# Kernel optimization log

Hardware: AMD Instinct MI355X
Metric: run time of the kernel (lower is better)

The kernel has to match this reference:

```python
import jax, jax.numpy as jnp
import numpy as np

B, N, E, T, HID = 8, 2048, 8192, 4096, 128
ALPHA_MAX = 0.05


def setup_inputs() -> dict:
    key = jax.random.key(0)
    k1, k2, k3, k4 = jax.random.split(key, 4)
    H = jax.random.normal(k1, (B, N, HID), dtype=jnp.float32)
    # Incidence-like matrices (dense in the original module)
    B1 = jax.random.normal(k2, (N, E), dtype=jnp.float32) * 0.05
    B2 = jax.random.normal(k3, (E, T), dtype=jnp.float32) * 0.05
    W = jax.random.normal(k4, (HID, HID), dtype=jnp.float32) * (1.0 / np.sqrt(HID))
    alpha_raw = jnp.asarray(-2.5, dtype=jnp.float32)
    return {"H": H, "B1": B1, "B2": B2, "W": W, "alpha_raw": alpha_raw}


def reference(H, B1, B2, W, alpha_raw):
    # diag(L1) = diag(B1^T B1) + diag(B2 B2^T) without forming [E,E]
    L1_diag = jnp.sum(B1 * B1, axis=0) + jnp.sum(B2 * B2, axis=1)  # [E]
    # nodes -> edges (B1_T @ H)
    E_feat = jnp.einsum('ne,bnh->beh', B1, H)          # [B,E,h]
    E_topo = E_feat * L1_diag[None, :, None]            # Laplacian-diag scale
    # edges -> nodes
    dH = jnp.einsum('ne,beh->bnh', B1, E_topo)          # [B,N,h]
    dH = jax.nn.relu(jnp.einsum('bnh,oh->bno', dH, W))  # Linear(no bias) + ReLU
    alpha = ALPHA_MAX * jax.nn.sigmoid(alpha_raw)
    return H + alpha * dH
```

## Files before the change

### kernel.cpp

```cpp
#include <hip/hip_runtime.h>
#include <hip/hip_bf16.h>

typedef unsigned short tcr_u16;
typedef unsigned int   tcr_u32;

enum TcrDims { kB = 8, kN = 2048, kE = 8192, kT = 4096, kHID = 128, kNC = 1024 };

union TcrFU { float f; tcr_u32 u; };

__device__ __forceinline__ float tcr_blo(tcr_u32 w) { TcrFU v; v.u = w << 16;          return v.f; }
__device__ __forceinline__ float tcr_bhi(tcr_u32 w) { TcrFU v; v.u = w & 0xFFFF0000u;  return v.f; }
__device__ __forceinline__ tcr_u16 tcr_f2b(float f) {
    TcrFU v; v.f = f; tcr_u32 x = v.u;
    return (tcr_u16)((x + 0x7FFFu + ((x >> 16) & 1u)) >> 16);
}
__device__ __forceinline__ tcr_u32 tcr_pk2(float lo, float hi) {
    __hip_bfloat16 a = __float2bfloat16(lo);
    __hip_bfloat16 b = __float2bfloat16(hi);
    tcr_u16 ua = *(const tcr_u16*)&a;
    tcr_u16 ub = *(const tcr_u16*)&b;
    return (tcr_u32)ua | ((tcr_u32)ub << 16);
}

struct alignas(8)  TcrU2 { tcr_u32 x, y; };
struct alignas(16) TcrU4 { tcr_u32 x, y, z, w; };
struct alignas(16) TcrF4 { float x, y, z, w; };

typedef __attribute__((ext_vector_type(8))) short bf16x8;
typedef __attribute__((ext_vector_type(4))) float f32x4;

template<int DT>
__device__ __forceinline__ void tcr_load4(const void* p, size_t idx, float* o) {
    if (DT == 0) {
        TcrU2 q = *(const TcrU2*)((const tcr_u16*)p + idx);
        o[0] = tcr_blo(q.x); o[1] = tcr_bhi(q.x);
        o[2] = tcr_blo(q.y); o[3] = tcr_bhi(q.y);
    } else {
        TcrF4 q = *(const TcrF4*)((const float*)p + idx);
        o[0] = q.x; o[1] = q.y; o[2] = q.z; o[3] = q.w;
    }
}

__global__ void TopoCycleResidualNodeAlpha_49641232007243_kernel() {}

__global__ void tcr_probe(const void* Hp, const void* Ap, int* flags) {
    if (blockIdx.x == 0 && threadIdx.x == 0) {
        const tcr_u32* w = (const tcr_u32*)Hp;
        int plausible = 0;
        for (int i = 0; i < 64; ++i) {
            float v = tcr_blo(w[i] & 0xFFFFu);
            float a = fabsf(v);
            if (a >= 0.015625f && a <= 8.0f) plausible++;
        }
        flags[0] = (plausible >= 32) ? 0 : 1;
        tcr_u32 aw = *(const tcr_u32*)Ap;
        flags[1] = (aw == 0xC0200000u) ? 1 : 0;
    }
}

template<int DT>
__global__ void tcr_l1_rowsum(const void* B2, float* L1, const int* flags) {
    if (flags[0] != DT) return;
    int e = blockIdx.x;
    size_t base = (size_t)e * kT;
    int t0 = threadIdx.x * 4;
    float s = 0.f;
    for (int it = 0; it < kT; it += 1024) {
        float v[4];
        tcr_load4<DT>(B2, base + it + t0, v);
        s += v[0] * v[0] + v[1] * v[1] + v[2] * v[2] + v[3] * v[3];
    }
    __shared__ float red[256];
    red[threadIdx.x] = s;
    __syncthreads();
    for (int off = 128; off > 0; off >>= 1) {
        if ((int)threadIdx.x < off) red[threadIdx.x] += red[threadIdx.x + off];
        __syncthreads();
    }
    if (threadIdx.x == 0) L1[e] = red[0];
}

template<int DT>
__global__ void tcr_l1_colsum(const void* B1, float* L1, const int* flags) {
    if (flags[0] != DT) return;
    int e0 = blockIdx.x * 1024 + threadIdx.x * 4;
    int n0 = blockIdx.y * 64;
    float s0 = 0, s1 = 0, s2 = 0, s3 = 0;
    for (int n = n0; n < n0 + 64; ++n) {
        float v[4];
        tcr_load4<DT>(B1, (size_t)n * kE + e0, v);
        s0 += v[0] * v[0]; s1 += v[1] * v[1]; s2 += v[2] * v[2]; s3 += v[3] * v[3];
    }
    atomicAdd(&L1[e0 + 0], s0);
    atomicAdd(&L1[e0 + 1], s1);
    atomicAdd(&L1[e0 + 2], s2);
    atomicAdd(&L1[e0 + 3], s3);
}

struct Reg8 { float f[8]; TcrU2 u0, u1; };

template<int DT>
__device__ __forceinline__ void load_T(const void* src, size_t base, int ld,
                                       Reg8* r, int t) {
    const int k  = (t & 15) * 2;
    const int c0 = (t >> 4) * 8;
    tcr_load4<DT>(src, base + (size_t)k * ld + c0,         r[0].f);
    tcr_load4<DT>(src, base + (size_t)k * ld + c0 + 4,     r[0].f + 4);
    tcr_load4<DT>(src, base + (size_t)(k + 1) * ld + c0,     r[1].f);
    tcr_load4<DT>(src, base + (size_t)(k + 1) * ld + c0 + 4, r[1].f + 4);
}

__device__ __forceinline__ void write_T(tcr_u16 (*dst)[40], const Reg8* r, int t) {
    const int k  = (t & 15) * 2;
    const int c0 = (t >> 4) * 8;
#pragma unroll
    for (int j = 0; j < 8; ++j)
        *(tcr_u32*)&dst[c0 + j][k] = tcr_pk2(r[0].f[j], r[1].f[j]);
}

template<int DT, int ROWS>
__device__ __forceinline__ void load_D(const void* src, size_t base, int ld,
                                       Reg8* r, int t) {
    const int k0 = (t & 3) * 8;
#pragma unroll
    for (int p = 0; p < ROWS / 64; ++p) {
        int m = (t >> 2) + p * 64;
        size_t off = base + (size_t)m * ld + k0;
        if (DT == 0) {
            r[p].u0 = *(const TcrU2*)((const tcr_u16*)src + off);
            r[p].u1 = *(const TcrU2*)((const tcr_u16*)src + off + 4);
        } else {
            tcr_load4<1>(src, off,     r[p].f);
            tcr_load4<1>(src, off + 4, r[p].f + 4);
        }
    }
}

template<int DT, int ROWS>
__device__ __forceinline__ void write_D(tcr_u16 (*dst)[40], const Reg8* r, int t) {
    const int k0 = (t & 3) * 8;
#pragma unroll
    for (int p = 0; p < ROWS / 64; ++p) {
        int m = (t >> 2) + p * 64;
        if (DT == 0) {
            *(TcrU2*)&dst[m][k0]     = r[p].u0;
            *(TcrU2*)&dst[m][k0 + 4] = r[p].u1;
        } else {
            TcrU2 o0, o1;
            o0.x = tcr_pk2(r[p].f[0], r[p].f[1]); o0.y = tcr_pk2(r[p].f[2], r[p].f[3]);
            o1.x = tcr_pk2(r[p].f[4], r[p].f[5]); o1.y = tcr_pk2(r[p].f[6], r[p].f[7]);
            *(TcrU2*)&dst[m][k0]     = o0;
            *(TcrU2*)&dst[m][k0 + 4] = o1;
        }
    }
}

template<int DT>
__global__ __launch_bounds__(256)
void tcr_mm1(const void* B1, const void* H, const float* L1,
             tcr_u16* C1T, const int* flags) {
    if (flags[0] != DT) return;
    __shared__ tcr_u16 As[128][40];
    __shared__ tcr_u16 Bs[128][40];
    const int t  = threadIdx.x;
    const int et = blockIdx.x * 128;
    const int ct = blockIdx.y * 128;
    const int b0 = ct >> 7;
    const int lane = t & 63, w = t >> 6;
    const int mf = lane & 15, q = lane >> 4;
    const int wr = w >> 1, wc = w & 1;

    const f32x4 zero4 = {0.f, 0.f, 0.f, 0.f};
    f32x4 acc[4][4];
#pragma unroll
    for (int i = 0; i < 4; ++i)
#pragma unroll
        for (int j = 0; j < 4; ++j) acc[i][j] = zero4;

    const size_t hbase = (size_t)b0 * ((size_t)kN * kHID);

    Reg8 ra[2], rb[2];
    load_T<DT>(B1, (size_t)0 * kE + et, kE, ra, t);
    load_T<DT>(H,  hbase,               kHID, rb, t);

    for (int kt = 0; kt < kN; kt += 32) {
        write_T(As, ra, t);
        write_T(Bs, rb, t);
        __syncthreads();
        if (kt + 32 < kN) {
            load_T<DT>(B1, (size_t)(kt + 32) * kE + et,        kE,   ra, t);
            load_T<DT>(H,  hbase + (size_t)(kt + 32) * kHID,   kHID, rb, t);
        }
        bf16x8 af[4], bf[4];
#pragma unroll
        for (int i = 0; i < 4; ++i)
            af[i] = *(const bf16x8*)&As[wr * 64 + i * 16 + mf][q * 8];
#pragma unroll
        for (int j = 0; j < 4; ++j)
            bf[j] = *(const bf16x8*)&Bs[wc * 64 + j * 16 + mf][q * 8];
#pragma unroll
        for (int i = 0; i < 4; ++i)
#pragma unroll
            for (int j = 0; j < 4; ++j)
                acc[i][j] = __builtin_amdgcn_mfma_f32_16x16x32_bf16(
                    af[i], bf[j], acc[i][j], 0, 0, 0);
        __syncthreads();
    }

#pragma unroll
    for (int i = 0; i < 4; ++i) {
        const int e0 = et + wr * 64 + i * 16 + q * 4;
        const TcrF4 s = *(const TcrF4*)&L1[e0];
#pragma unroll
        for (int j = 0; j < 4; ++j) {
            const int c = ct + wc * 64 + j * 16 + mf;
            f32x4 a = acc[i][j];
            TcrU2 o;
            o.x = tcr_pk2(a[0] * s.x, a[1] * s.y);
            o.y = tcr_pk2(a[2] * s.z, a[3] * s.w);
            *(TcrU2*)(C1T + (size_t)c * kE + e0) = o;
        }
    }
}

template<int DT>
__global__ __launch_bounds__(256)
void tcr_mm2(const void* B1, const tcr_u16* C1T, tcr_u16* dHp, int kper,
             const int* flags) {
    if (flags[0] != DT) return;
    __shared__ tcr_u16 As[64][40];
    __shared__ tcr_u16 Bs[128][40];
    const int t  = threadIdx.x;
    const int nt = blockIdx.x * 64;
    const int ct = blockIdx.y * 128;
    const int kbase = blockIdx.z * kper;
    const int lane = t & 63, w = t >> 6;
    const int mf = lane & 15, q = lane >> 4;
    const int wr = w >> 1, wc = w & 1;

    const f32x4 zero4 = {0.f, 0.f, 0.f, 0.f};
    f32x4 acc[2][4];
#pragma unroll
    for (int i = 0; i < 2; ++i)
#pragma unroll
        for (int j = 0; j < 4; ++j) acc[i][j] = zero4;

    Reg8 ra[1], rb[2];
    load_D<DT, 64>(B1,  (size_t)nt * kE + kbase, kE, ra, t);
    load_D<0, 128>(C1T, (size_t)ct * kE + kbase, kE, rb, t);

    for (int kt = 0; kt < kper; kt += 32) {
        write_D<DT, 64>(As, ra, t);
        write_D<0, 128>(Bs, rb, t);
        __syncthreads();
        if (kt + 32 < kper) {
            load_D<DT, 64>(B1,  (size_t)nt * kE + kbase + kt + 32, kE, ra, t);
            load_D<0, 128>(C1T, (size_t)ct * kE + kbase + kt + 32, kE, rb, t);
        }
        bf16x8 af[2], bf[4];
#pragma unroll
        for (int i = 0; i < 2; ++i)
            af[i] = *(const bf16x8*)&As[wr * 32 + i * 16 + mf][q * 8];
#pragma unroll
        for (int j = 0; j < 4; ++j)
            bf[j] = *(const bf16x8*)&Bs[wc * 64 + j * 16 + mf][q * 8];
#pragma unroll
        for (int i = 0; i < 2; ++i)
#pragma unroll
            for (int j = 0; j < 4; ++j)
                acc[i][j] = __builtin_amdgcn_mfma_f32_16x16x32_bf16(
                    af[i], bf[j], acc[i][j], 0, 0, 0);
        __syncthreads();
    }

    const int b0 = ct >> 7;
    tcr_u16* op = dHp + (size_t)blockIdx.z * ((size_t)kB * kN * kHID)
                + (size_t)b0 * kN * kHID;
#pragma unroll
    for (int i = 0; i < 2; ++i) {
        const int n0 = nt + wr * 32 + i * 16 + q * 4;
#pragma unroll
        for (int j = 0; j < 4; ++j) {
            const int h = wc * 64 + j * 16 + mf;
            f32x4 a = acc[i][j];
#pragma unroll
            for (int r = 0; r < 4; ++r)
                op[(size_t)(n0 + r) * kHID + h] = tcr_f2b(a[r]);
        }
    }
}

template<int DT>
__global__ __launch_bounds__(256)
void tcr_fuse2(const tcr_u16* dHp, int nparts, const void* H, const void* W,
               const void* Ap, void* outv, const int* flags) {
    if (flags[0] != DT) return;
    __shared__ tcr_u16 dhs[32][136];
    __shared__ tcr_u16 Ws[2][128][136];
    const int t  = threadIdx.x;
    const int r0 = blockIdx.x * 32;

    {
        const int r  = t >> 3;
        const int c0 = (t & 7) * 16;
        float s[16];
#pragma unroll
        for (int ii = 0; ii < 16; ++ii) s[ii] = 0.f;
        for (int p = 0; p < nparts; ++p) {
            const tcr_u16* src = dHp + (size_t)p * ((size_t)kB * kN * kHID)
                               + (size_t)(r0 + r) * kHID + c0;
            TcrU4 q0 = *(const TcrU4*)src;
            TcrU4 q1 = *(const TcrU4*)(src + 8);
            s[0] += tcr_blo(q0.x);  s[1] += tcr_bhi(q0.x);
            s[2] += tcr_blo(q0.y);  s[3] += tcr_bhi(q0.y);
            s[4] += tcr_blo(q0.z);  s[5] += tcr_bhi(q0.z);
            s[6] += tcr_blo(q0.w);  s[7] += tcr_bhi(q0.w);
            s[8] += tcr_blo(q1.x);  s[9] += tcr_bhi(q1.x);
            s[10] += tcr_blo(q1.y); s[11] += tcr_bhi(q1.y);
            s[12] += tcr_blo(q1.z); s[13] += tcr_bhi(q1.z);
            s[14] += tcr_blo(q1.w); s[15] += tcr_bhi(q1.w);
        }
#pragma unroll
        for (int ii = 0; ii < 16; ii += 2)
            *(tcr_u32*)&dhs[r][c0 + ii] = tcr_pk2(s[ii], s[ii + 1]);
    }

    {
        const int r  = t >> 1;
        const int c0 = (t & 1) * 64;
        if (DT == 0) {
            const tcr_u16* wsrc = (const tcr_u16*)W + (size_t)r * kHID + c0;
#pragma unroll
            for (int cc = 0; cc < 64; cc += 8)
                *(TcrU4*)&Ws[0][r][c0 + cc] = *(const TcrU4*)(wsrc + cc);
        } else {
            const float* wsrc = (const float*)W + (size_t)r * kHID + c0;
#pragma unroll
            for (int cc = 0; cc < 64; cc += 2) {
                float a = wsrc[cc], b = wsrc[cc + 1];
                tcr_u32 hi = tcr_pk2(a, b);
                tcr_u32 lo = tcr_pk2(a - tcr_blo(hi), b - tcr_bhi(hi));
                *(tcr_u32*)&Ws[0][r][c0 + cc] = hi;
                *(tcr_u32*)&Ws[1][r][c0 + cc] = lo;
            }
        }
    }
    __syncthreads();

    const int lane = t & 63, w = t >> 6;
    const int mf = lane & 15, q = lane >> 4;
    const f32x4 zero4 = {0.f, 0.f, 0.f, 0.f};
    f32x4 acc[2][2];
#pragma unroll
    for (int i = 0; i < 2; ++i)
#pragma unroll
        for (int j = 0; j < 2; ++j) acc[i][j] = zero4;

    const int NWP = (DT == 1) ? 2 : 1;
    for (int p = 0; p < NWP; ++p) {
#pragma unroll
        for (int ks = 0; ks < 4; ++ks) {
            bf16x8 af[2], bf[2];
#pragma unroll
            for (int i = 0; i < 2; ++i)
                af[i] = *(const bf16x8*)&dhs[i * 16 + mf][ks * 32 + q * 8];
#pragma unroll
            for (int j = 0; j < 2; ++j)
                bf[j] = *(const bf16x8*)&Ws[p][w * 32 + j * 16 + mf][ks * 32 + q * 8];
#pragma unroll
            for (int i = 0; i < 2; ++i)
#pragma unroll
                for (int j = 0; j < 2; ++j)
                    acc[i][j] = __builtin_amdgcn_mfma_f32_16x16x32_bf16(
                        af[i], bf[j], acc[i][j], 0, 0, 0);
        }
    }

    float araw;
    if (flags[1] == 1) araw = *(const float*)Ap;
    else               araw = tcr_blo((tcr_u32)(*(const tcr_u16*)Ap));
    const float alpha = 0.05f / (1.f + expf(-araw));

    float (*ot)[132] = (float(*)[132])&Ws[0][0][0];
    __syncthreads();
#pragma unroll
    for (int i = 0; i < 2; ++i) {
        const int rr = i * 16 + q * 4;
#pragma unroll
        for (int j = 0; j < 2; ++j) {
            const int o = w * 32 + j * 16 + mf;
            f32x4 a = acc[i][j];
#pragma unroll
            for (int r = 0; r < 4; ++r) {
                float v = a[r];
                ot[rr + r][o] = alpha * (v > 0.f ? v : 0.f);
            }
        }
    }
    __syncthreads();

    {
        const int r  = t >> 3;
        const int c0 = (t & 7) * 16;
        const size_t gbase = (size_t)(r0 + r) * kHID + c0;
        if (DT == 0) {
            const tcr_u16* hp = (const tcr_u16*)H + gbase;
            tcr_u16* op = (tcr_u16*)outv + gbase;
#pragma unroll
            for (int cc = 0; cc < 16; cc += 8) {
                TcrU4 hq = *(const TcrU4*)(hp + cc);
                TcrU4 oq;
                oq.x = tcr_pk2(tcr_blo(hq.x) + ot[r][c0 + cc + 0],
                               tcr_bhi(hq.x) + ot[r][c0 + cc + 1]);
                oq.y = tcr_pk2(tcr_blo(hq.y) + ot[r][c0 + cc + 2],
                               tcr_bhi(hq.y) + ot[r][c0 + cc + 3]);
                oq.z = tcr_pk2(tcr_blo(hq.z) + ot[r][c0 + cc + 4],
                               tcr_bhi(hq.z) + ot[r][c0 + cc + 5]);
                oq.w = tcr_pk2(tcr_blo(hq.w) + ot[r][c0 + cc + 6],
                               tcr_bhi(hq.w) + ot[r][c0 + cc + 7]);
                *(TcrU4*)(op + cc) = oq;
            }
        } else {
            const float* hp = (const float*)H + gbase;
            float* op = (float*)outv + gbase;
#pragma unroll
            for (int cc = 0; cc < 16; cc += 4) {
                TcrF4 hq = *(const TcrF4*)(hp + cc);
                TcrF4 oq;
                oq.x = hq.x + ot[r][c0 + cc + 0];
                oq.y = hq.y + ot[r][c0 + cc + 1];
                oq.z = hq.z + ot[r][c0 + cc + 2];
                oq.w = hq.w + ot[r][c0 + cc + 3];
                *(TcrF4*)(op + cc) = oq;
            }
        }
    }
}

extern "C" void kernel_launch(void* const* d_in, const int* in_sizes, int n_in,
                              void* d_out, int out_size, void* d_ws, size_t ws_size,
                              hipStream_t stream) {
    const void* Hp = 0; const void* B1p = 0; const void* B2p = 0;
    const void* Wp = 0; const void* Ap = 0;
    for (int i = 0; i < n_in; ++i) {
        switch (in_sizes[i]) {
            case 2097152:  Hp  = d_in[i]; break;
            case 16777216: B1p = d_in[i]; break;
            case 33554432: B2p = d_in[i]; break;
            case 16384:    Wp  = d_in[i]; break;
            case 1:        Ap  = d_in[i]; break;
            default: break;
        }
    }

    char* ws = (char*)d_ws;
    int*     flags = (int*)ws;
    tcr_u16* C1    = (tcr_u16*)(ws + 256);
    float*   L1    = (float*)(ws + 256 + (size_t)kE * kNC * 2);
    const size_t off_dHp = 256 + (size_t)kE * kNC * 2 + (size_t)kE * 4;
    tcr_u16* dHp   = (tcr_u16*)(ws + off_dHp);
    const size_t PS = (size_t)kB * kN * kHID;

    const int z = (ws_size >= off_dHp + 4 * PS * 2 + 1024) ? 4 : 2;
    const int kper = kE / z;

    tcr_probe<<<dim3(1), dim3(64), 0, stream>>>(Hp, Ap, flags);

    tcr_l1_rowsum<0><<<dim3(kE), dim3(256), 0, stream>>>(B2p, L1, flags);
    tcr_l1_rowsum<1><<<dim3(kE), dim3(256), 0, stream>>>(B2p, L1, flags);
    tcr_l1_colsum<0><<<dim3(8, 32), dim3(256), 0, stream>>>(B1p, L1, flags);
    tcr_l1_colsum<1><<<dim3(8, 32), dim3(256), 0, stream>>>(B1p, L1, flags);

    tcr_mm1<0><<<dim3(kE / 128, kNC / 128), dim3(256), 0, stream>>>(B1p, Hp, L1, C1, flags);
    tcr_mm1<1><<<dim3(kE / 128, kNC / 128), dim3(256), 0, stream>>>(B1p, Hp, L1, C1, flags);

    tcr_mm2<0><<<dim3(kN / 64, kNC / 128, z), dim3(256), 0, stream>>>(B1p, C1, dHp, kper, flags);
    tcr_mm2<1><<<dim3(kN / 64, kNC / 128, z), dim3(256), 0, stream>>>(B1p, C1, dHp, kper, flags);

    tcr_fuse2<0><<<dim3(512), dim3(256), 0, stream>>>(dHp, z, Hp, Wp, Ap, d_out, flags);
    tcr_fuse2<1><<<dim3(512), dim3(256), 0, stream>>>(dHp, z, Hp, Wp, Ap, d_out, flags);
}
```

Baseline: 448.9 us.

## Double-buffer LDS in GEMMs, shrink tiles, and merge dtype-dispatch kernel launches

The separate DT=0/DT=1 kernel launches are merged into single kernels that branch on the runtime dtype flag, halving the launch count. Both GEMM kernels now use double-buffered LDS with a single barrier per k-step. The next tile's global loads are issued before that barrier. Output tiles are narrowed from 128 to 64 columns, with launch_bounds raised for occupancy and the LDS row stride cut from 40 to 36 bf16. The tighter stride forces fragment loads to be split into two 8-byte reads, and the smaller tiles reduce per-block data reuse.

```diff
diff --git a/kernel.cpp b/kernel.cpp
--- a/kernel.cpp
+++ b/kernel.cpp
@@ -27,7 +27,10 @@
 struct alignas(16) TcrF4 { float x, y, z, w; };
 
 typedef __attribute__((ext_vector_type(8))) short bf16x8;
+typedef __attribute__((ext_vector_type(4))) short bf16x4;
 typedef __attribute__((ext_vector_type(4))) float f32x4;
+
+#define LDSW 36
 
 template<int DT>
 __device__ __forceinline__ void tcr_load4(const void* p, size_t idx, float* o) {
@@ -41,6 +44,15 @@
     }
 }
 
+__device__ __forceinline__ bf16x8 ld_frag(const tcr_u16* p) {
+    bf16x4 lo = *(const bf16x4*)p;
+    bf16x4 hi = *(const bf16x4*)(p + 4);
+    bf16x8 r;
+    r[0] = lo[0]; r[1] = lo[1]; r[2] = lo[2]; r[3] = lo[3];
+    r[4] = hi[0]; r[5] = hi[1]; r[6] = hi[2]; r[7] = hi[3];
+    return r;
+}
+
 __global__ void TopoCycleResidualNodeAlpha_49641232007243_kernel() {}
 
 __global__ void tcr_probe(const void* Hp, const void* Ap, int* flags) {
@@ -59,8 +71,7 @@
 }
 
 template<int DT>
-__global__ void tcr_l1_rowsum(const void* B2, float* L1, const int* flags) {
-    if (flags[0] != DT) return;
+__device__ __forceinline__ void rowsum_body(const void* B2, float* L1) {
     int e = blockIdx.x;
     size_t base = (size_t)e * kT;
     int t0 = threadIdx.x * 4;
@@ -80,9 +91,13 @@
     if (threadIdx.x == 0) L1[e] = red[0];
 }
 
-template<int DT>
-__global__ void tcr_l1_colsum(const void* B1, float* L1, const int* flags) {
-    if (flags[0] != DT) return;
+__global__ void tcr_l1_rowsum(const void* B2, float* L1, const int* flags) {
+    if (flags[0] == 0) rowsum_body<0>(B2, L1);
+    else               rowsum_body<1>(B2, L1);
+}
+
+template<int DT>
+__device__ __forceinline__ void colsum_body(const void* B1, float* L1) {
     int e0 = blockIdx.x * 1024 + threadIdx.x * 4;
     int n0 = blockIdx.y * 64;
     float s0 = 0, s1 = 0, s2 = 0, s3 = 0;
@@ -97,114 +112,111 @@
     atomicAdd(&L1[e0 + 3], s3);
 }
 
+__global__ void tcr_l1_colsum(const void* B1, float* L1, const int* flags) {
+    if (flags[0] == 0) colsum_body<0>(B1, L1);
+    else               colsum_body<1>(B1, L1);
+}
+
 struct Reg8 { float f[8]; TcrU2 u0, u1; };
 
-template<int DT>
+template<int DT, int CW>
 __device__ __forceinline__ void load_T(const void* src, size_t base, int ld,
                                        Reg8* r, int t) {
     const int k  = (t & 15) * 2;
-    const int c0 = (t >> 4) * 8;
-    tcr_load4<DT>(src, base + (size_t)k * ld + c0,         r[0].f);
-    tcr_load4<DT>(src, base + (size_t)k * ld + c0 + 4,     r[0].f + 4);
-    tcr_load4<DT>(src, base + (size_t)(k + 1) * ld + c0,     r[1].f);
-    tcr_load4<DT>(src, base + (size_t)(k + 1) * ld + c0 + 4, r[1].f + 4);
-}
-
-__device__ __forceinline__ void write_T(tcr_u16 (*dst)[40], const Reg8* r, int t) {
+    const int c0 = (t >> 4) * CW;
+    tcr_load4<DT>(src, base + (size_t)k * ld + c0, r[0].f);
+    if (CW == 8) tcr_load4<DT>(src, base + (size_t)k * ld + c0 + 4, r[0].f + 4);
+    tcr_load4<DT>(src, base + (size_t)(k + 1) * ld + c0, r[1].f);
+    if (CW == 8) tcr_load4<DT>(src, base + (size_t)(k + 1) * ld + c0 + 4, r[1].f + 4);
+}
+
+template<int CW>
+__device__ __forceinline__ void write_T(tcr_u16 (*dst)[LDSW], const Reg8* r, int t) {
     const int k  = (t & 15) * 2;
-    const int c0 = (t >> 4) * 8;
-#pragma unroll
-    for (int j = 0; j < 8; ++j)
+    const int c0 = (t >> 4) * CW;
+#pragma unroll
+    for (int j = 0; j < CW; ++j)
         *(tcr_u32*)&dst[c0 + j][k] = tcr_pk2(r[0].f[j], r[1].f[j]);
 }
 
-template<int DT, int ROWS>
-__device__ __forceinline__ void load_D(const void* src, size_t base, int ld,
-                                       Reg8* r, int t) {
-    const int k0 = (t & 3) * 8;
-#pragma unroll
-    for (int p = 0; p < ROWS / 64; ++p) {
-        int m = (t >> 2) + p * 64;
-        size_t off = base + (size_t)m * ld + k0;
-        if (DT == 0) {
-            r[p].u0 = *(const TcrU2*)((const tcr_u16*)src + off);
-            r[p].u1 = *(const TcrU2*)((const tcr_u16*)src + off + 4);
-        } else {
-            tcr_load4<1>(src, off,     r[p].f);
-            tcr_load4<1>(src, off + 4, r[p].f + 4);
-        }
-    }
-}
-
-template<int DT, int ROWS>
-__device__ __forceinline__ void write_D(tcr_u16 (*dst)[40], const Reg8* r, int t) {
-    const int k0 = (t & 3) * 8;
-#pragma unroll
-    for (int p = 0; p < ROWS / 64; ++p) {
-        int m = (t >> 2) + p * 64;
-        if (DT == 0) {
-            *(TcrU2*)&dst[m][k0]     = r[p].u0;
-            *(TcrU2*)&dst[m][k0 + 4] = r[p].u1;
-        } else {
-            TcrU2 o0, o1;
-            o0.x = tcr_pk2(r[p].f[0], r[p].f[1]); o0.y = tcr_pk2(r[p].f[2], r[p].f[3]);
-            o1.x = tcr_pk2(r[p].f[4], r[p].f[5]); o1.y = tcr_pk2(r[p].f[6], r[p].f[7]);
-            *(TcrU2*)&dst[m][k0]     = o0;
-            *(TcrU2*)&dst[m][k0 + 4] = o1;
-        }
-    }
-}
-
-template<int DT>
-__global__ __launch_bounds__(256)
-void tcr_mm1(const void* B1, const void* H, const float* L1,
-             tcr_u16* C1T, const int* flags) {
-    if (flags[0] != DT) return;
-    __shared__ tcr_u16 As[128][40];
-    __shared__ tcr_u16 Bs[128][40];
+template<int DT>
+__device__ __forceinline__ void load_D64(const void* src, size_t base, int ld,
+                                         Reg8& r, int t) {
+    const int m = t >> 2, k0 = (t & 3) * 8;
+    size_t off = base + (size_t)m * ld + k0;
+    if (DT == 0) {
+        r.u0 = *(const TcrU2*)((const tcr_u16*)src + off);
+        r.u1 = *(const TcrU2*)((const tcr_u16*)src + off + 4);
+    } else {
+        tcr_load4<1>(src, off,     r.f);
+        tcr_load4<1>(src, off + 4, r.f + 4);
+    }
+}
+
+template<int DT>
+__device__ __forceinline__ void write_D64(tcr_u16 (*dst)[LDSW], const Reg8& r, int t) {
+    const int m = t >> 2, k0 = (t & 3) * 8;
+    if (DT == 0) {
+        *(TcrU2*)&dst[m][k0]     = r.u0;
+        *(TcrU2*)&dst[m][k0 + 4] = r.u1;
+    } else {
+        TcrU2 o0, o1;
+        o0.x = tcr_pk2(r.f[0], r.f[1]); o0.y = tcr_pk2(r.f[2], r.f[3]);
+        o1.x = tcr_pk2(r.f[4], r.f[5]); o1.y = tcr_pk2(r.f[6], r.f[7]);
+        *(TcrU2*)&dst[m][k0]     = o0;
+        *(TcrU2*)&dst[m][k0 + 4] = o1;
+    }
+}
+
+template<int DT>
+__device__ void mm1_body(tcr_u16 (*As)[128][LDSW], tcr_u16 (*Bs)[64][LDSW],
+                         const void* B1, const void* H, const float* L1,
+                         tcr_u16* C1T) {
     const int t  = threadIdx.x;
     const int et = blockIdx.x * 128;
-    const int ct = blockIdx.y * 128;
+    const int ct = blockIdx.y * 64;
     const int b0 = ct >> 7;
+    const int h0 = ct & 127;
     const int lane = t & 63, w = t >> 6;
     const int mf = lane & 15, q = lane >> 4;
     const int wr = w >> 1, wc = w & 1;
 
     const f32x4 zero4 = {0.f, 0.f, 0.f, 0.f};
-    f32x4 acc[4][4];
+    f32x4 acc[4][2];
 #pragma unroll
     for (int i = 0; i < 4; ++i)
 #pragma unroll
-        for (int j = 0; j < 4; ++j) acc[i][j] = zero4;
-
-    const size_t hbase = (size_t)b0 * ((size_t)kN * kHID);
+        for (int j = 0; j < 2; ++j) acc[i][j] = zero4;
+
+    const size_t hoff = (size_t)b0 * ((size_t)kN * kHID) + h0;
 
     Reg8 ra[2], rb[2];
-    load_T<DT>(B1, (size_t)0 * kE + et, kE, ra, t);
-    load_T<DT>(H,  hbase,               kHID, rb, t);
-
+    load_T<DT, 8>(B1, et, kE, ra, t);
+    load_T<DT, 4>(H, hoff, kHID, rb, t);
+
+    int p = 0;
     for (int kt = 0; kt < kN; kt += 32) {
-        write_T(As, ra, t);
-        write_T(Bs, rb, t);
+        write_T<8>(As[p], ra, t);
+        write_T<4>(Bs[p], rb, t);
+        if (kt + 32 < kN) {
+            load_T<DT, 8>(B1, (size_t)(kt + 32) * kE + et, kE, ra, t);
+            load_T<DT, 4>(H, hoff + (size_t)(kt + 32) * kHID, kHID, rb, t);
+        }
         __syncthreads();
-        if (kt + 32 < kN) {
-            load_T<DT>(B1, (size_t)(kt + 32) * kE + et,        kE,   ra, t);
-            load_T<DT>(H,  hbase + (size_t)(kt + 32) * kHID,   kHID, rb, t);
-        }
-        bf16x8 af[4], bf[4];
+        bf16x8 af[4], bf[2];
 #pragma unroll
         for (int i = 0; i < 4; ++i)
-            af[i] = *(const bf16x8*)&As[wr * 64 + i * 16 + mf][q * 8];
-#pragma unroll
-        for (int j = 0; j < 4; ++j)
-            bf[j] = *(const bf16x8*)&Bs[wc * 64 + j * 16 + mf][q * 8];
+            af[i] = ld_frag(&As[p][wr * 64 + i * 16 + mf][q * 8]);
+#pragma unroll
+        for (int j = 0; j < 2; ++j)
+            bf[j] = ld_frag(&Bs[p][wc * 32 + j * 16 + mf][q * 8]);
 #pragma unroll
         for (int i = 0; i < 4; ++i)
 #pragma unroll
-            for (int j = 0; j < 4; ++j)
+            for (int j = 0; j < 2; ++j)
                 acc[i][j] = __builtin_amdgcn_mfma_f32_16x16x32_bf16(
                     af[i], bf[j], acc[i][j], 0, 0, 0);
-        __syncthreads();
+        p ^= 1;
     }
 
 #pragma unroll
@@ -212,8 +224,8 @@
         const int e0 = et + wr * 64 + i * 16 + q * 4;
         const TcrF4 s = *(const TcrF4*)&L1[e0];
 #pragma unroll
-        for (int j = 0; j < 4; ++j) {
-            const int c = ct + wc * 64 + j * 16 + mf;
+        for (int j = 0; j < 2; ++j) {
+            const int c = ct + wc * 32 + j * 16 + mf;
             f32x4 a = acc[i][j];
             TcrU2 o;
             o.x = tcr_pk2(a[0] * s.x, a[1] * s.y);
@@ -223,65 +235,73 @@
     }
 }
 
-template<int DT>
-__global__ __launch_bounds__(256)
-void tcr_mm2(const void* B1, const tcr_u16* C1T, tcr_u16* dHp, int kper,
+__global__ __launch_bounds__(256, 4)
+void tcr_mm1(const void* B1, const void* H, const float* L1, tcr_u16* C1T,
              const int* flags) {
-    if (flags[0] != DT) return;
-    __shared__ tcr_u16 As[64][40];
-    __shared__ tcr_u16 Bs[128][40];
+    __shared__ tcr_u16 As[2][128][LDSW];
+    __shared__ tcr_u16 Bs[2][64][LDSW];
+    if (flags[0] == 0) mm1_body<0>(As, Bs, B1, H, L1, C1T);
+    else               mm1_body<1>(As, Bs, B1, H, L1, C1T);
+}
+
+template<int DT>
+__device__ void mm2_body(tcr_u16 (*As)[64][LDSW], tcr_u16 (*Bs)[64][LDSW],
+                         const void* B1, const tcr_u16* C1T, tcr_u16* dHp,
+                         int kper) {
     const int t  = threadIdx.x;
     const int nt = blockIdx.x * 64;
-    const int ct = blockIdx.y * 128;
+    const int ct = blockIdx.y * 64;
     const int kbase = blockIdx.z * kper;
     const int lane = t & 63, w = t >> 6;
     const int mf = lane & 15, q = lane >> 4;
     const int wr = w >> 1, wc = w & 1;
 
     const f32x4 zero4 = {0.f, 0.f, 0.f, 0.f};
-    f32x4 acc[2][4];
+    f32x4 acc[2][2];
 #pragma unroll
     for (int i = 0; i < 2; ++i)
 #pragma unroll
-        for (int j = 0; j < 4; ++j) acc[i][j] = zero4;
-
-    Reg8 ra[1], rb[2];
-    load_D<DT, 64>(B1,  (size_t)nt * kE + kbase, kE, ra, t);
-    load_D<0, 128>(C1T, (size_t)ct * kE + kbase, kE, rb, t);
-
+        for (int j = 0; j < 2; ++j) acc[i][j] = zero4;
+
+    Reg8 ra, rb;
+    load_D64<DT>(B1,  (size_t)nt * kE + kbase, kE, ra, t);
+    load_D64<0>(C1T, (size_t)ct * kE + kbase, kE, rb, t);
+
+    int p = 0;
     for (int kt = 0; kt < kper; kt += 32) {
-        write_D<DT, 64>(As, ra, t);
-        write_D<0, 128>(Bs, rb, t);
+        write_D64<DT>(As[p], ra, t);
+        write_D64<0>(Bs[p], rb, t);
+        if (kt + 32 < kper) {
+            load_D64<DT>(B1,  (size_t)nt * kE + kbase + kt + 32, kE, ra, t);
+            load_D64<0>(C1T, (size_t)ct * kE + kbase + kt + 32, kE, rb, t);
+        }
         __syncthreads();
-        if (kt + 32 < kper) {
-            load_D<DT, 64>(B1,  (size_t)nt * kE + kbase + kt + 32, kE, ra, t);
-            load_D<0, 128>(C1T, (size_t)ct * kE + kbase + kt + 32, kE, rb, t);
-        }
-        bf16x8 af[2], bf[4];
+        bf16x8 af[2], bf[2];
 #pragma unroll
         for (int i = 0; i < 2; ++i)
-            af[i] = *(const bf16x8*)&As[wr * 32 + i * 16 + mf][q * 8];
-#pragma unroll
-        for (int j = 0; j < 4; ++j)
-            bf[j] = *(const bf16x8*)&Bs[wc * 64 + j * 16 + mf][q * 8];
+            af[i] = ld_frag(&As[p][wr * 32 + i * 16 + mf][q * 8]);
+#pragma unroll
+        for (int j = 0; j < 2; ++j)
+            bf[j] = ld_frag(&Bs[p][wc * 32 + j * 16 + mf][q * 8]);
 #pragma unroll
         for (int i = 0; i < 2; ++i)
 #pragma unroll
-            for (int j = 0; j < 4; ++j)
+            for (int j = 0; j < 2; ++j)
                 acc[i][j] = __builtin_amdgcn_mfma_f32_16x16x32_bf16(
                     af[i], bf[j], acc[i][j], 0, 0, 0);
-        __syncthreads();
+        p ^= 1;
     }
 
     const int b0 = ct >> 7;
+    const int h0 = ct & 127;
     tcr_u16* op = dHp + (size_t)blockIdx.z * ((size_t)kB * kN * kHID)
                 + (size_t)b0 * kN * kHID;
 #pragma unroll
     for (int i = 0; i < 2; ++i) {
         const int n0 = nt + wr * 32 + i * 16 + q * 4;
 #pragma unroll
-        for (int j = 0; j < 4; ++j) {
-            const int h = wc * 64 + j * 16 + mf;
+        for (int j = 0; j < 2; ++j) {
+            const int h = h0 + wc * 32 + j * 16 + mf;
             f32x4 a = acc[i][j];
 #pragma unroll
             for (int r = 0; r < 4; ++r)
@@ -290,13 +310,21 @@
     }
 }
 
-template<int DT>
-__global__ __launch_bounds__(256)
-void tcr_fuse2(const tcr_u16* dHp, int nparts, const void* H, const void* W,
-               const void* Ap, void* outv, const int* flags) {
-    if (flags[0] != DT) return;
-    __shared__ tcr_u16 dhs[32][136];
-    __shared__ tcr_u16 Ws[2][128][136];
+__global__ __launch_bounds__(256, 4)
+void tcr_mm2(const void* B1, const tcr_u16* C1T, tcr_u16* dHp, int kper,
+             const int* flags) {
+    __shared__ tcr_u16 As[2][64][LDSW];
+    __shared__ tcr_u16 Bs[2][64][LDSW];
+    if (flags[0] == 0) mm2_body<0>(As, Bs, B1, C1T, dHp, kper);
+    else               mm2_body<1>(As, Bs, B1, C1T, dHp, kper);
+}
+
+template<int DT>
+__device__ void fuse2_body(tcr_u16 (*dhs)[136], tcr_u16 (*WsA)[136],
+                           tcr_u16 (*WsB)[136],
+                           const tcr_u16* dHp, int nparts, const void* H,
+                           const void* W, const void* Ap, void* outv,
+                           const int* flags) {
     const int t  = threadIdx.x;
     const int r0 = blockIdx.x * 32;
 
@@ -332,7 +360,7 @@
             const tcr_u16* wsrc = (const tcr_u16*)W + (size_t)r * kHID + c0;
 #pragma unroll
             for (int cc = 0; cc < 64; cc += 8)
-                *(TcrU4*)&Ws[0][r][c0 + cc] = *(const TcrU4*)(wsrc + cc);
+                *(TcrU4*)&WsA[r][c0 + cc] = *(const TcrU4*)(wsrc + cc);
         } else {
             const float* wsrc = (const float*)W + (size_t)r * kHID + c0;
 #pragma unroll
@@ -340,8 +368,8 @@
                 float a = wsrc[cc], b = wsrc[cc + 1];
                 tcr_u32 hi = tcr_pk2(a, b);
                 tcr_u32 lo = tcr_pk2(a - tcr_blo(hi), b - tcr_bhi(hi));
-                *(tcr_u32*)&Ws[0][r][c0 + cc] = hi;
-                *(tcr_u32*)&Ws[1][r][c0 + cc] = lo;
+                *(tcr_u32*)&WsA[r][c0 + cc] = hi;
+                *(tcr_u32*)&WsB[r][c0 + cc] = lo;
             }
         }
     }
@@ -358,6 +386,7 @@
 
     const int NWP = (DT == 1) ? 2 : 1;
     for (int p = 0; p < NWP; ++p) {
+        tcr_u16 (*Wp_)[136] = (p == 0) ? WsA : WsB;
 #pragma unroll
         for (int ks = 0; ks < 4; ++ks) {
             bf16x8 af[2], bf[2];
@@ -366,7 +395,7 @@
                 af[i] = *(const bf16x8*)&dhs[i * 16 + mf][ks * 32 + q * 8];
 #pragma unroll
             for (int j = 0; j < 2; ++j)
-                bf[j] = *(const bf16x8*)&Ws[p][w * 32 + j * 16 + mf][ks * 32 + q * 8];
+                bf[j] = *(const bf16x8*)&Wp_[w * 32 + j * 16 + mf][ks * 32 + q * 8];
 #pragma unroll
             for (int i = 0; i < 2; ++i)
 #pragma unroll
@@ -381,7 +410,7 @@
     else               araw = tcr_blo((tcr_u32)(*(const tcr_u16*)Ap));
     const float alpha = 0.05f / (1.f + expf(-araw));
 
-    float (*ot)[132] = (float(*)[132])&Ws[0][0][0];
+    float (*ot)[132] = (float(*)[132])&WsA[0][0];
     __syncthreads();
 #pragma unroll
     for (int i = 0; i < 2; ++i) {
@@ -437,6 +466,18 @@
     }
 }
 
+__global__ __launch_bounds__(256)
+void tcr_fuse2(const tcr_u16* dHp, int nparts, const void* H, const void* W,
+               const void* Ap, void* outv, const int* flags) {
+    __shared__ tcr_u16 dhs[32][136];
+    __shared__ tcr_u16 WsA[128][136];
+    __shared__ tcr_u16 WsB[128][136];
+    if (flags[0] == 0)
+        fuse2_body<0>(dhs, WsA, WsB, dHp, nparts, H, W, Ap, outv, flags);
+    else
+        fuse2_body<1>(dhs, WsA, WsB, dHp, nparts, H, W, Ap, outv, flags);
+}
+
 extern "C" void kernel_launch(void* const* d_in, const int* in_sizes, int n_in,
                               void* d_out, int out_size, void* d_ws, size_t ws_size,
                               hipStream_t stream) {
@@ -466,17 +507,12 @@
 
     tcr_probe<<<dim3(1), dim3(64), 0, stream>>>(Hp, Ap, flags);
 
-    tcr_l1_rowsum<0><<<dim3(kE), dim3(256), 0, stream>>>(B2p, L1, flags);
-    tcr_l1_rowsum<1><<<dim3(kE), dim3(256), 0, stream>>>(B2p, L1, flags);
-    tcr_l1_colsum<0><<<dim3(8, 32), dim3(256), 0, stream>>>(B1p, L1, flags);
-    tcr_l1_colsum<1><<<dim3(8, 32), dim3(256), 0, stream>>>(B1p, L1, flags);
-
-    tcr_mm1<0><<<dim3(kE / 128, kNC / 128), dim3(256), 0, stream>>>(B1p, Hp, L1, C1, flags);
-    tcr_mm1<1><<<dim3(kE / 128, kNC / 128), dim3(256), 0, stream>>>(B1p, Hp, L1, C1, flags);
-
-    tcr_mm2<0><<<dim3(kN / 64, kNC / 128, z), dim3(256), 0, stream>>>(B1p, C1, dHp, kper, flags);
-    tcr_mm2<1><<<dim3(kN / 64, kNC / 128, z), dim3(256), 0, stream>>>(B1p, C1, dHp, kper, flags);
-
-    tcr_fuse2<0><<<dim3(512), dim3(256), 0, stream>>>(dHp, z, Hp, Wp, Ap, d_out, flags);
-    tcr_fuse2<1><<<dim3(512), dim3(256), 0, stream>>>(dHp, z, Hp, Wp, Ap, d_out, flags);
-}
+    tcr_l1_rowsum<<<dim3(kE), dim3(256), 0, stream>>>(B2p, L1, flags);
+    tcr_l1_colsum<<<dim3(8, 32), dim3(256), 0, stream>>>(B1p, L1, flags);
+
+    tcr_mm1<<<dim3(kE / 128, kNC / 64), dim3(256), 0, stream>>>(B1p, Hp, L1, C1, flags);
+
+    tcr_mm2<<<dim3(kN / 64, kNC / 64, z), dim3(256), 0, stream>>>(B1p, C1, dHp, kper, flags);
+
+    tcr_fuse2<<<dim3(512), dim3(256), 0, stream>>>(dHp, z, Hp, Wp, Ap, d_out, flags);
+}
```

Result: slower. 527.5 us (+17.5%).
